# Performance work log

Hardware: AMD Instinct MI355X
Metric: run time of the kernel (lower is better)

## Reference

```python
import jax, jax.numpy as jnp
import numpy as np
from jax import lax

VOCAB = 28996  # bert-base-cased vocab size (static for segment_sum)
B, S, D = 32, 512, 768
NUM_CLASSES = 9


def _lstm_dir(x, w_ih, w_hh, b_ih, b_hh):
    # x: [T, N, In]; torch gate order i, f, g, o packed along dim 0 of weights
    T, N, _ = x.shape
    H = w_hh.shape[1]
    xg = jnp.einsum('tni,gi->tng', x, w_ih) + b_ih  # precompute input projections [T,N,4H]

    def step(carry, xg_t):
        h, c = carry
        g = xg_t + h @ w_hh.T + b_hh
        i, f, gg, o = jnp.split(g, 4, axis=-1)
        c = jax.nn.sigmoid(f) * c + jax.nn.sigmoid(i) * jnp.tanh(gg)
        h = jax.nn.sigmoid(o) * jnp.tanh(c)
        return (h, c), h

    h0 = jnp.zeros((N, H), x.dtype)
    _, ys = lax.scan(step, (h0, h0), xg)
    return ys  # [T, N, H]


def setup_inputs() -> dict:
    key = jax.random.key(0)
    ks = jax.random.split(key, 8)
    H, In = D, 2 * D
    w = 0.02
    return {
        'batch': jax.random.randint(ks[0], (B, S), 0, VOCAB),
        'hidden': jax.random.normal(ks[1], (B, S, D), jnp.float32),
        'w_ih_f': jax.random.normal(ks[2], (4 * H, In), jnp.float32) * w,
        'w_hh_f': jax.random.normal(ks[3], (4 * H, H), jnp.float32) * w,
        'b_ih_f': jnp.zeros((4 * H,), jnp.float32),
        'b_hh_f': jnp.zeros((4 * H,), jnp.float32),
        'w_ih_b': jax.random.normal(ks[4], (4 * H, In), jnp.float32) * w,
        'w_hh_b': jax.random.normal(ks[5], (4 * H, H), jnp.float32) * w,
        'b_ih_b': jnp.zeros((4 * H,), jnp.float32),
        'b_hh_b': jnp.zeros((4 * H,), jnp.float32),
        'lin_w': jax.random.normal(ks[6], (NUM_CLASSES, 2 * H), jnp.float32) * w,
        'lin_b': jnp.zeros((NUM_CLASSES,), jnp.float32),
    }


def reference(batch, hidden, w_ih_f, w_hh_f, b_ih_f, b_hh_f,
              w_ih_b, w_hh_b, b_ih_b, b_hh_b, lin_w, lin_b):
    b, s, d = hidden.shape
    flat_ids = batch.reshape(-1)            # [B*S]
    flat_h = hidden.reshape(-1, d)          # [B*S, D]
    # segment mean of embeddings grouped by raw token id (the dict loop in torch)
    sums = jax.ops.segment_sum(flat_h, flat_ids, num_segments=VOCAB)
    counts = jax.ops.segment_sum(jnp.ones((flat_ids.shape[0], 1), hidden.dtype),
                                 flat_ids, num_segments=VOCAB)
    means = sums / jnp.maximum(counts, 1.0)
    ctx = means[flat_ids].reshape(b, s, d)  # gather-broadcast back per position
    x = jnp.concatenate([hidden, ctx], axis=2)  # [B, S, 2D]
    # nn.LSTM is not batch_first: scans over dim0 (B acts as time, S as batch)
    out_f = _lstm_dir(x, w_ih_f, w_hh_f, b_ih_f, b_hh_f)
    out_b = _lstm_dir(x[::-1], w_ih_b, w_hh_b, b_ih_b, b_hh_b)[::-1]
    out = jnp.concatenate([out_f, out_b], axis=-1)  # [B, S, 2D]
    # dropout is identity in eval mode
    return out @ lin_w.T + lin_b  # [B, S, num_classes]
```

## Files before the change

kernel.cpp:

```cpp
#include <hip/hip_runtime.h>

#define VOCAB 28996
#define BB 32
#define SS 512
#define DD 768
#define NCLS 9
#define ROWS (BB*SS)
#define IN2 (2*DD)
#define G4 (4*DD)
#define NB2 (2*G4)

typedef __attribute__((ext_vector_type(8))) short short8;
typedef __attribute__((ext_vector_type(4))) short shortx4;
typedef __attribute__((ext_vector_type(4))) float floatx4;
typedef unsigned long long ull;

__device__ __forceinline__ float bf2f(unsigned short u){
  union { unsigned int i; float f; } v; v.i = ((unsigned int)u) << 16; return v.f;
}
__device__ __forceinline__ unsigned short f2bf(float f){
  union { float f; unsigned int i; } v; v.f = f;
  unsigned int r = v.i + 0x7FFFu + ((v.i >> 16) & 1u);
  return (unsigned short)(r >> 16);
}
__device__ __forceinline__ float sigf(float x){ return 1.0f / (1.0f + __expf(-x)); }
__device__ __forceinline__ float tanhfast(float x){
  float y = fminf(fmaxf(x, -15.f), 15.f);
  float e = __expf(2.f * y);
  return 1.f - 2.f / (e + 1.f);
}

__device__ __forceinline__ void gl_lds16(const unsigned short* g, unsigned short* l){
  __builtin_amdgcn_global_load_lds((__attribute__((address_space(1))) void*)(g),
                                   (__attribute__((address_space(3))) void*)(l), 16, 0, 0);
}
template<int LOCAL>
__device__ __forceinline__ void gl_lds16_h(const unsigned short* g, unsigned short* l){
  __builtin_amdgcn_global_load_lds((__attribute__((address_space(1))) void*)(g),
                                   (__attribute__((address_space(3))) void*)(l), 16, 0,
                                   LOCAL ? 1 : 17);
}
__device__ __forceinline__ void store16_sc1(unsigned short* p, short8 v){
  asm volatile("global_store_dwordx4 %0, %1, off sc0 sc1" :: "v"(p), "v"(v) : "memory");
}

#define VMCNT(n) do { asm volatile("s_waitcnt vmcnt(" #n ")" ::: "memory"); \
                      __builtin_amdgcn_sched_barrier(0); } while (0)

__global__ void seg_scatter(const int* __restrict__ ids, const float* __restrict__ hidden,
                            float* __restrict__ sums, float* __restrict__ counts)
{
  int r = blockIdx.x;
  int id = ids[r];
  const float* h = hidden + (long)r * DD;
  float* s = sums + (long)id * DD;
  for (int d = threadIdx.x; d < DD; d += 256)
    atomicAdd(&s[d], h[d]);
  if (threadIdx.x == 0) atomicAdd(&counts[id], 1.0f);
}

__global__ void build_x(const int* __restrict__ ids, const float* __restrict__ hidden,
                        const float* __restrict__ sums, const float* __restrict__ counts,
                        unsigned short* __restrict__ x)
{
  int r = blockIdx.x;
  int id = ids[r];
  float inv = 1.0f / fmaxf(counts[id], 1.0f);
  const float* h = hidden + (long)r * DD;
  const float* s = sums + (long)id * DD;
  unsigned short* xr = x + (long)r * IN2;
  for (int d = threadIdx.x; d < DD; d += 256) {
    xr[d]      = f2bf(h[d]);
    xr[DD + d] = f2bf(s[d] * inv);
  }
}

__global__ void conv_w_perm(const float* __restrict__ w, unsigned short* __restrict__ o, int K)
{
  long i = (long)blockIdx.x * 256 + threadIdx.x;
  if (i >= (long)G4 * K) return;
  int row = (int)(i / K); int k = (int)(i - (long)row * K);
  int u = row >> 2, g = row & 3;
  o[i] = f2bf(w[((long)(g * DD + u)) * K + k]);
}

__global__ void conv_bias_perm(const float* __restrict__ bif, const float* __restrict__ bhf,
                               const float* __restrict__ bib, const float* __restrict__ bhb,
                               float* __restrict__ o)
{
  int n = blockIdx.x * 256 + threadIdx.x;
  if (n >= NB2) return;
  int d = n / G4, rr = n - d * G4, u = rr >> 2, g = rr & 3;
  int s = g * DD + u;
  o[n] = d ? (bib[s] + bhb[s]) : (bif[s] + bhf[s]);
}

__global__ __launch_bounds__(512, 1)
void gemm_bt256(const unsigned short* __restrict__ A, int lda,
                const unsigned short* __restrict__ B, int ldb,
                unsigned short* __restrict__ C, int ldc,
                const float* __restrict__ bias, int K)
{
  __shared__ unsigned short lA[2][16384];
  __shared__ unsigned short lB[2][16384];
  const int t = threadIdx.x;
  const int lane = t & 63;
  const int wv = t >> 6;
  const int wm = wv >> 1;
  const int wn = wv & 1;
  const int l15 = lane & 15, q = lane >> 4;
  const long m0 = (long)blockIdx.x * 256;
  const long n0 = (long)blockIdx.y * 256;
  const int rs  = t >> 2;
  const int sc  = (((t & 3) ^ ((t >> 3) & 3))) * 8;
  const int qsw = (q ^ ((l15 >> 1) & 3)) * 8;

  const unsigned short* gA = A + (m0 + rs) * (long)lda + sc;
  const unsigned short* gB = B + (n0 + rs) * (long)ldb + sc;
  const long a128 = (long)128 * lda;
  const long b128 = (long)128 * ldb;

  #define PIECE(b, kt, p, hf) do {                                               \
    const long kb_ = (long)(kt) * 64 + (p) * 32;                                 \
    gl_lds16(gA + kb_ + (hf) * a128, &lA[b][(p) * 8192 + (hf) * 4096 + t * 8]);  \
    gl_lds16(gB + kb_ + (hf) * b128, &lB[b][(p) * 8192 + (hf) * 4096 + t * 8]);  \
  } while (0)

  floatx4 acc[4][8];
  #pragma unroll
  for (int i = 0; i < 4; i++)
    #pragma unroll
    for (int j = 0; j < 8; j++)
      acc[i][j] = (floatx4){0.f, 0.f, 0.f, 0.f};

  PIECE(0, 0, 0, 0); PIECE(0, 0, 0, 1);
  PIECE(0, 0, 1, 0); PIECE(0, 0, 1, 1);

  #pragma unroll 2
  for (int kt = 0; kt < 24; kt++) {
    const int cur = kt & 1;
    const int nxt = cur ^ 1;
    const unsigned short* pA = &lA[cur][0];
    const unsigned short* pB = &lB[cur][0];

    VMCNT(4);
    __builtin_amdgcn_s_barrier();

    #pragma unroll
    for (int ks = 0; ks < 2; ks++) {
      short8 bfr[8];
      #pragma unroll
      for (int ih = 0; ih < 2; ih++) {
        if (kt < 23) {
          if (ks == 0 && ih == 0) PIECE(nxt, kt + 1, 0, 0);
          if (ks == 0 && ih == 1) PIECE(nxt, kt + 1, 0, 1);
          if (ks == 1 && ih == 0) PIECE(nxt, kt + 1, 1, 0);
          if (ks == 1 && ih == 1) PIECE(nxt, kt + 1, 1, 1);
        }
        if (ih == 0) {
          #pragma unroll
          for (int j = 0; j < 8; j++)
            bfr[j] = *(const short8*)(pB + ks * 8192 + (wn * 128 + j * 16 + l15) * 32 + qsw);
        }
        short8 af[2];
        #pragma unroll
        for (int ii = 0; ii < 2; ii++)
          af[ii] = *(const short8*)(pA + ks * 8192 + (wm * 64 + (ih * 2 + ii) * 16 + l15) * 32 + qsw);
        __builtin_amdgcn_s_setprio(1);
        #pragma unroll
        for (int ii = 0; ii < 2; ii++)
          #pragma unroll
          for (int j = 0; j < 8; j++)
            acc[ih * 2 + ii][j] =
              __builtin_amdgcn_mfma_f32_16x16x32_bf16(af[ii], bfr[j], acc[ih * 2 + ii][j], 0, 0, 0);
        __builtin_amdgcn_s_setprio(0);
      }
      if (ks == 0) {
        if (kt < 23) VMCNT(4); else VMCNT(0);
        __builtin_amdgcn_s_barrier();
      }
    }
  }
  #undef PIECE

  #pragma unroll
  for (int i = 0; i < 4; i++) {
    #pragma unroll
    for (int j = 0; j < 8; j++) {
      const long mg = m0 + wm * 64 + i * 16 + q * 4;
      const long ng = n0 + wn * 128 + j * 16 + l15;
      const float bb = bias[ng];
      #pragma unroll
      for (int r = 0; r < 4; r++)
        C[(mg + r) * (long)ldc + ng] = f2bf(acc[i][j][r] + bb);
    }
  }
}

template<int LOCAL>
__global__ __launch_bounds__(512, 1)
void lstm_persist(const unsigned short* __restrict__ xg, int ldxg,
                  const unsigned short* __restrict__ whh,
                  unsigned short* __restrict__ hbuf,
                  unsigned short* __restrict__ outc,
                  unsigned* bar,
                  int dir0, int ndir)
{
  __shared__ unsigned short bufA[2][16384];
  __shared__ unsigned short bufB[2][16384];
  __shared__ unsigned short hout[128 * 40];

  const int bid = blockIdx.x;
  int dm, nt;
  if (LOCAL) { dm = bid & 7; nt = bid >> 3; }
  else { int xcd = bid & 7; int idx = bid >> 3;
         dm = idx & 3; nt = (idx >> 2) * 8 + xcd; }
  const int ld  = (ndir == 2) ? (dm & 1) : 0;
  const int dir = dir0 + ld;
  const int mt  = (ndir == 2) ? (dm >> 1) : dm;
  const int m0 = mt * 128, n0 = nt * 128;
  const int u0 = n0 >> 2;
  unsigned* gbar = bar + dm * 16;
  const int nb24 = 24;

  const int t0 = threadIdx.x;
  const int lane = t0 & 63;
  const int wv = t0 >> 6;
  const int wm = wv >> 1;
  const int wn = wv & 1;
  const int l15 = lane & 15, q = lane >> 4;
  const long ldoff = (ndir == 2 && ld == 1) ? (long)G4 : 0;

  const unsigned short* Bdir = whh + (long)dir * G4 * DD;
  const int srow  = lane >> 2;
  const int scolA = (((lane & 3) ^ ((lane >> 3) & 3))) * 8;
  const int qsw   = (q ^ ((l15 >> 1) & 3)) * 8;

  const int rb = wv * 16 + srow;
  const unsigned short* wB  = Bdir + (long)(n0 + rb) * DD + scolA;
  const unsigned short* hA0 = hbuf + ((long)0 * ndir + ld) * ((long)SS * DD) + (long)(m0 + rb) * DD + scolA;
  const unsigned short* hA1 = hbuf + ((long)1 * ndir + ld) * ((long)SS * DD) + (long)(m0 + rb) * DD + scolA;

  float c_reg[2][4];
  #pragma unroll
  for (int i = 0; i < 2; i++)
    #pragma unroll
    for (int j = 0; j < 4; j++)
      c_reg[i][j] = 0.f;

  for (int s = 0; s < BB; s++) {
    const int tt = dir ? (BB - 1 - s) : s;
    const unsigned short* hA = (s & 1) ? hA1 : hA0;
    unsigned short* hw = hbuf + (((long)((s + 1) & 1)) * ndir + ld) * ((long)SS * DD);

    #pragma unroll
    for (int p = 0; p < 4; p++) {
      gl_lds16_h<LOCAL>(hA + p * 32, &bufA[0][p * 4096 + wv * 512 + lane * 8]);
      gl_lds16         (wB + p * 32, &bufB[0][p * 4096 + wv * 512 + lane * 8]);
    }
    shortx4 xr0[4], xr1[4];
    {
      const unsigned short* xb = xg + ((long)tt * SS + m0) * ldxg + ldoff + n0;
      const unsigned short* xb0 = xb + (long)(wm * 32 + l15) * ldxg + wn * 64 + q * 4;
      const unsigned short* xb1 = xb0 + (long)16 * ldxg;
      #pragma unroll
      for (int j = 0; j < 4; j++) {
        xr0[j] = *(const shortx4*)(xb0 + j * 16);
        xr1[j] = *(const shortx4*)(xb1 + j * 16);
      }
    }

    floatx4 acc[2][4];
    #pragma unroll
    for (int i = 0; i < 2; i++)
      #pragma unroll
      for (int j = 0; j < 4; j++)
        acc[i][j] = (floatx4){0.f, 0.f, 0.f, 0.f};

    #pragma unroll
    for (int j6 = 0; j6 < 6; j6++) {
      if (j6 < 5) {
        const int b = (j6 + 1) & 1;
        const long kb = (long)(j6 + 1) * 128;
        #pragma unroll
        for (int p = 0; p < 4; p++) {
          gl_lds16_h<LOCAL>(hA + kb + p * 32, &bufA[b][p * 4096 + wv * 512 + lane * 8]);
          gl_lds16         (wB + kb + p * 32, &bufB[b][p * 4096 + wv * 512 + lane * 8]);
        }
      }
      if (j6 == 0)      VMCNT(16);
      else if (j6 < 5)  VMCNT(8);
      else              VMCNT(0);
      __builtin_amdgcn_s_barrier();
      const int b = j6 & 1;
      __builtin_amdgcn_s_setprio(1);
      #pragma unroll
      for (int ks = 0; ks < 4; ks++) {
        const unsigned short* pA = &bufA[b][ks * 4096];
        const unsigned short* pB = &bufB[b][ks * 4096];
        short8 af[2], bfr[4];
        #pragma unroll
        for (int i = 0; i < 2; i++)
          af[i] = *(const short8*)(pA + (wm * 32 + i * 16 + l15) * 32 + qsw);
        #pragma unroll
        for (int j = 0; j < 4; j++)
          bfr[j] = *(const short8*)(pB + (wn * 64 + j * 16 + l15) * 32 + qsw);
        #pragma unroll
        for (int i = 0; i < 2; i++)
          #pragma unroll
          for (int j = 0; j < 4; j++)
            acc[i][j] = __builtin_amdgcn_mfma_f32_16x16x32_bf16(bfr[j], af[i], acc[i][j], 0, 0, 0);
      }
      __builtin_amdgcn_s_setprio(0);
      if (j6 < 5) __builtin_amdgcn_s_barrier();
    }

    #pragma unroll
    for (int i = 0; i < 2; i++) {
      const int mrow = wm * 32 + i * 16 + l15;
      #pragma unroll
      for (int j = 0; j < 4; j++) {
        const int nb = wn * 64 + j * 16 + q * 4;
        shortx4 xv = i ? xr1[j] : xr0[j];
        float gi = acc[i][j][0] + bf2f((unsigned short)xv[0]);
        float gf = acc[i][j][1] + bf2f((unsigned short)xv[1]);
        float gg = acc[i][j][2] + bf2f((unsigned short)xv[2]);
        float go = acc[i][j][3] + bf2f((unsigned short)xv[3]);
        float c = sigf(gf) * c_reg[i][j] + sigf(gi) * tanhfast(gg);
        float h = sigf(go) * tanhfast(c);
        c_reg[i][j] = c;
        hout[mrow * 40 + (nb >> 2)] = f2bf(h);
      }
    }
    __syncthreads();
    {
      const int row = t0 >> 2;
      const int qq = t0 & 3;
      short8 v0 = *(const short8*)(hout + row * 40 + qq * 8);
      unsigned short* hwp = hw + (long)(m0 + row) * DD + u0 + qq * 8;
      unsigned short* op  = outc + ((long)tt * SS + m0 + row) * IN2 + dir * DD + u0 + qq * 8;
      if (LOCAL) *(short8*)hwp = v0;
      else       store16_sc1(hwp, v0);
      *(short8*)op = v0;
    }
    if (s < BB - 1) {
      VMCNT(0);
      __builtin_amdgcn_s_barrier();
      if (threadIdx.x == 0) {
        unsigned g = __hip_atomic_load(gbar + 1, __ATOMIC_RELAXED, __HIP_MEMORY_SCOPE_AGENT);
        unsigned a = __hip_atomic_fetch_add(gbar, 1u, __ATOMIC_RELAXED, __HIP_MEMORY_SCOPE_AGENT);
        if (a == (unsigned)(nb24 - 1)) {
          __hip_atomic_store(gbar, 0u, __ATOMIC_RELAXED, __HIP_MEMORY_SCOPE_AGENT);
          __hip_atomic_store(gbar + 1, g + 1u, __ATOMIC_RELEASE, __HIP_MEMORY_SCOPE_AGENT);
        } else {
          unsigned curv;
          do {
            __builtin_amdgcn_s_sleep(2);
            curv = __hip_atomic_load(gbar + 1, __ATOMIC_RELAXED, __HIP_MEMORY_SCOPE_AGENT);
          } while (curv == g);
        }
      }
      __builtin_amdgcn_s_barrier();
    }
  }
}

__global__ void final_linear(const unsigned short* __restrict__ xin, const float* __restrict__ w,
                             const float* __restrict__ b, float* __restrict__ out)
{
  __shared__ float red[NCLS * 256];
  int row = blockIdx.x;
  const unsigned short* x = xin + (long)row * IN2;
  float p[NCLS];
  #pragma unroll
  for (int c = 0; c < NCLS; c++) p[c] = 0.f;
  for (int k = threadIdx.x; k < IN2; k += 256) {
    float xv = bf2f(x[k]);
    #pragma unroll
    for (int c = 0; c < NCLS; c++) p[c] += xv * w[c * IN2 + k];
  }
  #pragma unroll
  for (int c = 0; c < NCLS; c++) red[c * 256 + threadIdx.x] = p[c];
  __syncthreads();
  for (int s = 128; s > 0; s >>= 1) {
    if (threadIdx.x < s) {
      #pragma unroll
      for (int c = 0; c < NCLS; c++)
        red[c * 256 + threadIdx.x] += red[c * 256 + threadIdx.x + s];
    }
    __syncthreads();
  }
  if (threadIdx.x < NCLS)
    out[(long)row * NCLS + threadIdx.x] = red[threadIdx.x * 256] + b[threadIdx.x];
}

extern "C" void kernel_launch(void* const* d_in, const int* in_sizes, int n_in,
                              void* d_out, int out_size, void* d_ws, size_t ws_size,
                              hipStream_t stream)
{
  const int*   batch  = (const int*)d_in[0];
  const float* hidden = (const float*)d_in[1];
  const float* w_ih_f = (const float*)d_in[2];
  const float* w_hh_f = (const float*)d_in[3];
  const float* b_ih_f = (const float*)d_in[4];
  const float* b_hh_f = (const float*)d_in[5];
  const float* w_ih_b = (const float*)d_in[6];
  const float* w_hh_b = (const float*)d_in[7];
  const float* b_ih_b = (const float*)d_in[8];
  const float* b_hh_b = (const float*)d_in[9];
  const float* lin_w  = (const float*)d_in[10];
  const float* lin_b  = (const float*)d_in[11];
  float* out = (float*)d_out;

  char* ws = (char*)d_ws;
  size_t off = 0;
  auto alloc = [&](size_t bytes) -> char* {
    char* p = ws + off;
    off += (bytes + 255) & ~(size_t)255;
    return p;
  };

  const size_t SZ_XG_A = (size_t)ROWS * NB2 * 2;
  const size_t SZ_XG_B = (size_t)ROWS * G4  * 2;
  const size_t SZ_XBF  = (size_t)ROWS * IN2 * 2;
  const size_t SZ_W    = (size_t)G4 * IN2 * 2;
  const size_t SZ_BIAS = (size_t)NB2 * 4;
  const size_t SZ_HBUF = (size_t)2 * 2 * SS * DD * 2;
  const size_t SZ_BAR  = 512;
  const size_t SZ_SUMS = (size_t)VOCAB * DD * 4 + (size_t)VOCAB * 4;

  const size_t NEED_C = SZ_XG_A + SZ_XBF + SZ_W + SZ_BIAS + SZ_HBUF + SZ_BAR + 8 * 256;
  const bool combined = ws_size >= NEED_C;

  const long nWIH = (long)G4 * IN2;
  const long nWHH = (long)G4 * DD;

  if (combined) {
    unsigned short* xg   = (unsigned short*)alloc(SZ_XG_A);
    unsigned short* xbf  = (unsigned short*)alloc(SZ_XBF);
    unsigned short* wbuf = (unsigned short*)alloc(SZ_W);
    float*          bias = (float*)alloc(SZ_BIAS);
    unsigned short* hbuf = (unsigned short*)alloc(SZ_HBUF);
    unsigned*       bar  = (unsigned*)alloc(SZ_BAR);
    float* sums   = (float*)xg;
    float* counts = sums + (size_t)VOCAB * DD;

    hipMemsetAsync(sums, 0, SZ_SUMS, stream);
    hipMemsetAsync(bar, 0, SZ_BAR, stream);
    seg_scatter<<<ROWS, 256, 0, stream>>>(batch, hidden, sums, counts);
    build_x<<<ROWS, 256, 0, stream>>>(batch, hidden, sums, counts, xbf);
    conv_bias_perm<<<(NB2 + 255) / 256, 256, 0, stream>>>(b_ih_f, b_hh_f, b_ih_b, b_hh_b, bias);

    for (int dir = 0; dir < 2; dir++) {
      conv_w_perm<<<(unsigned)((nWIH + 255) / 256), 256, 0, stream>>>(dir ? w_ih_b : w_ih_f, wbuf, IN2);
      dim3 grid(ROWS / 256, G4 / 256, 1);
      gemm_bt256<<<grid, 512, 0, stream>>>(xbf, IN2, wbuf, IN2,
                                           xg + (size_t)dir * G4, NB2,
                                           bias + (size_t)dir * G4, IN2);
    }
    conv_w_perm<<<(unsigned)((nWHH + 255) / 256), 256, 0, stream>>>(w_hh_f, wbuf, DD);
    conv_w_perm<<<(unsigned)((nWHH + 255) / 256), 256, 0, stream>>>(w_hh_b, wbuf + (size_t)G4 * DD, DD);

    hipMemsetAsync(hbuf, 0, SZ_HBUF, stream);
    lstm_persist<1><<<192, 512, 0, stream>>>(xg, NB2, wbuf, hbuf, xbf, bar, 0, 2);
    final_linear<<<ROWS, 256, 0, stream>>>(xbf, lin_w, lin_b, out);
  } else {
    unsigned short* xg   = (unsigned short*)alloc(SZ_XG_B);
    unsigned short* xbf  = (unsigned short*)alloc(SZ_XBF);
    unsigned short* outc = (unsigned short*)alloc(SZ_XBF);
    unsigned short* wih  = (unsigned short*)alloc(SZ_W);
    unsigned short* whh  = (unsigned short*)alloc(SZ_W);
    float*          bias = (float*)alloc(SZ_BIAS);
    unsigned short* hbuf = (unsigned short*)alloc(SZ_HBUF);
    unsigned*       bar  = (unsigned*)alloc(SZ_BAR);
    float* sums   = (float*)xg;
    float* counts = sums + (size_t)VOCAB * DD;

    hipMemsetAsync(sums, 0, SZ_SUMS, stream);
    hipMemsetAsync(bar, 0, SZ_BAR, stream);
    seg_scatter<<<ROWS, 256, 0, stream>>>(batch, hidden, sums, counts);
    build_x<<<ROWS, 256, 0, stream>>>(batch, hidden, sums, counts, xbf);
    conv_bias_perm<<<(NB2 + 255) / 256, 256, 0, stream>>>(b_ih_f, b_hh_f, b_ih_b, b_hh_b, bias);
    conv_w_perm<<<(unsigned)((nWHH + 255) / 256), 256, 0, stream>>>(w_hh_f, whh, DD);
    conv_w_perm<<<(unsigned)((nWHH + 255) / 256), 256, 0, stream>>>(w_hh_b, whh + (size_t)G4 * DD, DD);

    for (int dir = 0; dir < 2; dir++) {
      conv_w_perm<<<(unsigned)((nWIH + 255) / 256), 256, 0, stream>>>(dir ? w_ih_b : w_ih_f, wih, IN2);
      {
        dim3 grid(ROWS / 256, G4 / 256, 1);
        gemm_bt256<<<grid, 512, 0, stream>>>(xbf, IN2, wih, IN2, xg, G4,
                                             bias + (size_t)dir * G4, IN2);
      }
      hipMemsetAsync(hbuf, 0, SZ_HBUF, stream);
      lstm_persist<0><<<96, 512, 0, stream>>>(xg, G4, whh, hbuf, outc, bar, dir, 1);
    }
    final_linear<<<ROWS, 256, 0, stream>>>(outc, lin_w, lin_b, out);
  }
}
```

Baseline: 1.136 ms.

## Triple-buffer LSTM recurrent GEMM and prefetch weights across grid barrier

Splits the persistent LSTM step's K loop into 12 smaller 64-wide chunks with a 3-stage LDS ring, issuing loads two chunks ahead. This drops the second barrier per chunk and keeps more loads in flight. The first two W_hh chunks for the next timestep are issued before the inter-block spin barrier, so weight loads overlap the grid sync. It also uses nontemporal loads for xg and nontemporal stores for the output. The cost is more barriers per step and finer-grained vmcnt accounting, which has to match the number of loads issued.

```diff
diff --git a/kernel.cpp b/kernel.cpp
--- a/kernel.cpp
+++ b/kernel.cpp
@@ -206,8 +206,8 @@
                   unsigned* bar,
                   int dir0, int ndir)
 {
-  __shared__ unsigned short bufA[2][16384];
-  __shared__ unsigned short bufB[2][16384];
+  __shared__ unsigned short bufA[3][8192];
+  __shared__ unsigned short bufB[3][8192];
   __shared__ unsigned short hout[128 * 40];
 
   const int bid = blockIdx.x;
@@ -241,6 +241,13 @@
   const unsigned short* hA0 = hbuf + ((long)0 * ndir + ld) * ((long)SS * DD) + (long)(m0 + rb) * DD + scolA;
   const unsigned short* hA1 = hbuf + ((long)1 * ndir + ld) * ((long)SS * DD) + (long)(m0 + rb) * DD + scolA;
 
+  #define STAGE_B(j, b) do { const long kb_ = (long)(j) * 64;                 \
+    gl_lds16(wB + kb_,      &bufB[b][wv * 512 + lane * 8]);                   \
+    gl_lds16(wB + kb_ + 32, &bufB[b][4096 + wv * 512 + lane * 8]); } while (0)
+  #define STAGE_A(j, b) do { const long kb_ = (long)(j) * 64;                 \
+    gl_lds16_h<LOCAL>(hA + kb_,      &bufA[b][wv * 512 + lane * 8]);          \
+    gl_lds16_h<LOCAL>(hA + kb_ + 32, &bufA[b][4096 + wv * 512 + lane * 8]); } while (0)
+
   float c_reg[2][4];
   #pragma unroll
   for (int i = 0; i < 2; i++)
@@ -253,22 +260,20 @@
     const unsigned short* hA = (s & 1) ? hA1 : hA0;
     unsigned short* hw = hbuf + (((long)((s + 1) & 1)) * ndir + ld) * ((long)SS * DD);
 
-    #pragma unroll
-    for (int p = 0; p < 4; p++) {
-      gl_lds16_h<LOCAL>(hA + p * 32, &bufA[0][p * 4096 + wv * 512 + lane * 8]);
-      gl_lds16         (wB + p * 32, &bufB[0][p * 4096 + wv * 512 + lane * 8]);
-    }
+    if (s == 0) { STAGE_B(0, 0); STAGE_B(1, 1); }
     shortx4 xr0[4], xr1[4];
     {
       const unsigned short* xb = xg + ((long)tt * SS + m0) * ldxg + ldoff + n0;
       const unsigned short* xb0 = xb + (long)(wm * 32 + l15) * ldxg + wn * 64 + q * 4;
       const unsigned short* xb1 = xb0 + (long)16 * ldxg;
       #pragma unroll
-      for (int j = 0; j < 4; j++) {
-        xr0[j] = *(const shortx4*)(xb0 + j * 16);
-        xr1[j] = *(const shortx4*)(xb1 + j * 16);
-      }
-    }
+      for (int jj = 0; jj < 4; jj++) {
+        xr0[jj] = __builtin_nontemporal_load((const shortx4*)(xb0 + jj * 16));
+        xr1[jj] = __builtin_nontemporal_load((const shortx4*)(xb1 + jj * 16));
+      }
+    }
+    STAGE_A(0, 0);
+    STAGE_A(1, 1);
 
     floatx4 acc[2][4];
     #pragma unroll
@@ -278,24 +283,20 @@
         acc[i][j] = (floatx4){0.f, 0.f, 0.f, 0.f};
 
     #pragma unroll
-    for (int j6 = 0; j6 < 6; j6++) {
-      if (j6 < 5) {
-        const int b = (j6 + 1) & 1;
-        const long kb = (long)(j6 + 1) * 128;
-        #pragma unroll
-        for (int p = 0; p < 4; p++) {
-          gl_lds16_h<LOCAL>(hA + kb + p * 32, &bufA[b][p * 4096 + wv * 512 + lane * 8]);
-          gl_lds16         (wB + kb + p * 32, &bufB[b][p * 4096 + wv * 512 + lane * 8]);
-        }
-      }
-      if (j6 == 0)      VMCNT(16);
-      else if (j6 < 5)  VMCNT(8);
-      else              VMCNT(0);
+    for (int j12 = 0; j12 < 12; j12++) {
+      if (j12 == 0)       VMCNT(2);
+      else if (j12 < 11)  VMCNT(4);
+      else                VMCNT(0);
       __builtin_amdgcn_s_barrier();
-      const int b = j6 & 1;
+      if (j12 < 10) {
+        const int bn = (j12 + 2) % 3;
+        STAGE_B(j12 + 2, bn);
+        STAGE_A(j12 + 2, bn);
+      }
+      const int b = j12 % 3;
       __builtin_amdgcn_s_setprio(1);
       #pragma unroll
-      for (int ks = 0; ks < 4; ks++) {
+      for (int ks = 0; ks < 2; ks++) {
         const unsigned short* pA = &bufA[b][ks * 4096];
         const unsigned short* pB = &bufB[b][ks * 4096];
         short8 af[2], bfr[4];
@@ -312,7 +313,6 @@
             acc[i][j] = __builtin_amdgcn_mfma_f32_16x16x32_bf16(bfr[j], af[i], acc[i][j], 0, 0, 0);
       }
       __builtin_amdgcn_s_setprio(0);
-      if (j6 < 5) __builtin_amdgcn_s_barrier();
     }
 
     #pragma unroll
@@ -341,11 +341,13 @@
       unsigned short* op  = outc + ((long)tt * SS + m0 + row) * IN2 + dir * DD + u0 + qq * 8;
       if (LOCAL) *(short8*)hwp = v0;
       else       store16_sc1(hwp, v0);
-      *(short8*)op = v0;
+      __builtin_nontemporal_store(v0, (short8*)op);
     }
     if (s < BB - 1) {
       VMCNT(0);
       __builtin_amdgcn_s_barrier();
+      STAGE_B(0, 0);
+      STAGE_B(1, 1);
       if (threadIdx.x == 0) {
         unsigned g = __hip_atomic_load(gbar + 1, __ATOMIC_RELAXED, __HIP_MEMORY_SCOPE_AGENT);
         unsigned a = __hip_atomic_fetch_add(gbar, 1u, __ATOMIC_RELAXED, __HIP_MEMORY_SCOPE_AGENT);
@@ -363,6 +365,8 @@
       __builtin_amdgcn_s_barrier();
     }
   }
+  #undef STAGE_A
+  #undef STAGE_B
 }
 
 __global__ void final_linear(const unsigned short* __restrict__ xin, const float* __restrict__ w,
```

After: 1.111 ms. 1.02x faster.
